# Kernel tuning notes

Measured on AMD Instinct MI355X. Metric: run time of the kernel, lower is better.

## Reference

```python
import jax, jax.numpy as jnp
import numpy as np

B, CDD, L, T, H, NH = 16, 10, 64, 128, 768, 12
DH = H // NH          # head dim = 64
S = CDD * L + T       # full sequence = 768 (640 candidate tokens + 128 terms)


def setup_inputs() -> dict:
    key = jax.random.key(0)
    ks = jax.random.split(key, 7)
    w = 0.02
    return {
        "hidden_states": jax.random.normal(ks[0], (B, S, H), jnp.float32),
        "Wq": jax.random.normal(ks[1], (H, H), jnp.float32) * w,
        "bq": jax.random.normal(ks[2], (H,), jnp.float32) * w,
        "Wk": jax.random.normal(ks[3], (H, H), jnp.float32) * w,
        "bk": jax.random.normal(ks[4], (H,), jnp.float32) * w,
        "Wv": jax.random.normal(ks[5], (H, H), jnp.float32) * w,
        "bv": jax.random.normal(ks[6], (H,), jnp.float32) * w,
    }


def _one_pass_mask(dtype):
    # block-diagonal over candidates + dense global columns for terms
    block = jnp.kron(jnp.eye(CDD, dtype=dtype), jnp.ones((L, L), dtype=dtype))  # [CDD*L, CDD*L]
    return jnp.concatenate([block, jnp.ones((CDD * L, T), dtype=dtype)], axis=-1)  # [CDD*L, S]


def reference(hidden_states, Wq, bq, Wk, bk, Wv, bv):
    def split_heads(x):  # [B, s, H] -> [B, NH, s, DH]
        return x.reshape(B, -1, NH, DH).transpose(0, 2, 1, 3)

    attn_field = hidden_states[:, :-T]                     # [B, CDD*L, H] queries only
    q = split_heads(attn_field @ Wq.T + bq)                # [B, NH, CDD*L, DH]
    k = split_heads(hidden_states @ Wk.T + bk)             # [B, NH, S, DH]
    v = split_heads(hidden_states @ Wv.T + bv)             # [B, NH, S, DH]

    mask = _one_pass_mask(q.dtype)                         # [CDD*L, S]
    scale = 1.0 / np.sqrt(DH).astype(np.float32)
    # NOTE: original multiplies scores by the mask (masked entries become 0, not -inf)
    scores = jnp.einsum('bhqd,bhkd->bhqk', q, k) * scale * mask
    probs = jax.nn.softmax(scores, axis=-1)                # [B, NH, CDD*L, S]

    ctx = jnp.einsum('bhqk,bhkd->bhqd', probs, v)          # [B, NH, CDD*L, DH]
    ctx = jnp.concatenate([ctx, v[:, :, -T:]], axis=2)     # append term values untouched
    return ctx.transpose(0, 2, 1, 3).reshape(B, S, H)
```

## Files before the change

### kernel.cpp

```cpp
#include <hip/hip_runtime.h>

constexpr int Bb  = 16;
constexpr int CDD = 10;
constexpr int Lc  = 64;
constexpr int T   = 128;
constexpr int H   = 768;
constexpr int NH  = 12;
constexpr int DH  = 64;
constexpr int S   = 768;
constexpr int SQ  = 640;
constexpr int MROWS = Bb * S;

typedef __attribute__((ext_vector_type(8))) short bf16x8;
typedef __attribute__((ext_vector_type(4))) short bf16x4;
typedef __attribute__((ext_vector_type(4))) float f32x4;

__device__ inline unsigned short f2bf(float f) {
  unsigned u = __float_as_uint(f);
  u += 0x7fff + ((u >> 16) & 1);
  return (unsigned short)(u >> 16);
}
__device__ inline float bf2f(unsigned short h) {
  return __uint_as_float(((unsigned)h) << 16);
}

__device__ inline void gld_lds16(const void* g, void* l) {
  __builtin_amdgcn_global_load_lds(
      (const __attribute__((address_space(1))) void*)g,
      (__attribute__((address_space(3))) void*)l, 16, 0, 0);
}

__device__ inline bf16x8 ld_b64x2(const unsigned short* p) {
  union { bf16x8 v; bf16x4 h[2]; } u;
  u.h[0] = *(const bf16x4*)p;
  u.h[1] = *(const bf16x4*)(p + 4);
  return u.v;
}

constexpr int NX4 = MROWS * H / 4;
constexpr int NW4 = H * H / 4;
__global__ void convert_all(const float* __restrict__ X,
                            const float* __restrict__ Wq,
                            const float* __restrict__ Wk,
                            const float* __restrict__ Wv,
                            unsigned short* __restrict__ Xb,
                            unsigned short* __restrict__ Wb,
                            float* __restrict__ part) {
  int i = blockIdx.x * blockDim.x + threadIdx.x;
  if (i < Bb * H) part[i] = 0.f;
  const int stride = gridDim.x * blockDim.x;
  const int total = NX4 + 3 * NW4;
  for (; i < total; i += stride) {
    const float* src;
    unsigned short* dst;
    int off;
    if (i < NX4) {
      src = X; dst = Xb; off = i;
    } else {
      int k = i - NX4;
      int w = k / NW4;
      off = k - w * NW4;
      src = (w == 0) ? Wq : (w == 1) ? Wk : Wv;
      dst = Wb + (size_t)w * H * H;
    }
    float4 v = ((const float4*)src)[off];
    ushort4 o;
    o.x = f2bf(v.x); o.y = f2bf(v.y); o.z = f2bf(v.z); o.w = f2bf(v.w);
    ((ushort4*)dst)[off] = o;
  }
}

__launch_bounds__(256, 4)
__global__ void qkv_gemm(const unsigned short* __restrict__ Xb,
                         const unsigned short* __restrict__ Wb,
                         const float* __restrict__ bq, const float* __restrict__ bk,
                         const float* __restrict__ bv,
                         unsigned short* __restrict__ Qb, unsigned short* __restrict__ Kb,
                         unsigned short* __restrict__ Vb,
                         float* __restrict__ part,
                         float* __restrict__ out) {
  const int z = blockIdx.z;
  if (z == 0 && (blockIdx.x % 6) == 5) return;
  const unsigned short* W = Wb + (size_t)z * H * H;
  const float* bias = (z == 0) ? bq : (z == 1) ? bk : bv;
  unsigned short* Y = (z == 0) ? Qb : (z == 1) ? Kb : Vb;

  const int i0 = blockIdx.x * 128;
  const int j0 = blockIdx.y * 128;
  const int tid = threadIdx.x;
  const int wave = tid >> 6, lane = tid & 63;
  const int wr = wave >> 1, wc = wave & 1;
  const int col = lane & 15, quad = lane >> 4;

  __shared__ unsigned short As[128 * 64];
  __shared__ unsigned short Bs[128 * 64];

  f32x4 acc[4][4];
#pragma unroll
  for (int i = 0; i < 4; i++)
#pragma unroll
    for (int j = 0; j < 4; j++) acc[i][j] = (f32x4){0.f, 0.f, 0.f, 0.f};

  int rS[4], gcS[4];
#pragma unroll
  for (int i = 0; i < 4; i++) {
    int s = tid + 256 * i;
    rS[i] = s >> 3;
    gcS[i] = (s & 7) ^ (rS[i] & 7);
  }

  for (int kt = 0; kt < 12; kt++) {
    const int k0 = kt * 64;
#pragma unroll
    for (int i = 0; i < 4; i++)
      gld_lds16(Xb + (size_t)(i0 + rS[i]) * H + k0 + gcS[i] * 8, &As[(tid + 256 * i) * 8]);
#pragma unroll
    for (int i = 0; i < 4; i++)
      gld_lds16(W + (size_t)(j0 + rS[i]) * H + k0 + gcS[i] * 8, &Bs[(tid + 256 * i) * 8]);
    __builtin_amdgcn_s_waitcnt(0);
    __syncthreads();

#pragma unroll
    for (int h = 0; h < 2; h++) {
      bf16x8 a[4], b[4];
#pragma unroll
      for (int mt = 0; mt < 4; mt++) {
        int r = wr * 64 + mt * 16 + col;
        a[mt] = *(const bf16x8*)&As[r * 64 + (((h * 4 + quad) ^ (r & 7)) * 8)];
      }
#pragma unroll
      for (int nt = 0; nt < 4; nt++) {
        int r = wc * 64 + nt * 16 + col;
        b[nt] = *(const bf16x8*)&Bs[r * 64 + (((h * 4 + quad) ^ (r & 7)) * 8)];
      }
#pragma unroll
      for (int mt = 0; mt < 4; mt++)
#pragma unroll
        for (int nt = 0; nt < 4; nt++)
          acc[mt][nt] = __builtin_amdgcn_mfma_f32_16x16x32_bf16(a[mt], b[nt], acc[mt][nt], 0, 0, 0);
    }
    __syncthreads();
  }

  float colsum[4] = {0.f, 0.f, 0.f, 0.f};
#pragma unroll
  for (int mt = 0; mt < 4; mt++) {
#pragma unroll
    for (int nt = 0; nt < 4; nt++) {
      const int j = j0 + wc * 64 + nt * 16 + col;
      const float bj = bias[j];
#pragma unroll
      for (int r = 0; r < 4; r++) {
        const int i = i0 + wr * 64 + mt * 16 + quad * 4 + r;
        const float v = acc[mt][nt][r] + bj;
        Y[(size_t)i * H + j] = f2bf(v);
        if (z == 2) {
          colsum[nt] += v;
          int s = i - (i / S) * S;
          if (s >= SQ) out[(size_t)i * H + j] = v;
        }
      }
    }
  }
  if (z == 2) {
    const int b = blockIdx.x / 6;
#pragma unroll
    for (int nt = 0; nt < 4; nt++) {
      float s = colsum[nt];
      s += __shfl_xor(s, 16, 64);
      s += __shfl_xor(s, 32, 64);
      if (quad == 0) {
        const int j = j0 + wc * 64 + nt * 16 + col;
        atomicAdd(&part[b * H + j], s);
      }
    }
  }
}

__launch_bounds__(256, 3)
__global__ void attn_kernel(const unsigned short* __restrict__ Qb,
                            const unsigned short* __restrict__ Kb,
                            const unsigned short* __restrict__ Vb,
                            const float* __restrict__ part,
                            float* __restrict__ out) {
  const int g = blockIdx.x;
  const int bid = (g & 7) * 240 + (g >> 3);
  const int c = bid % CDD;
  const int h = (bid / CDD) % NH;
  const int b = bid / (CDD * NH);
  const int tid = threadIdx.x;
  const int wave = tid >> 6, lane = tid & 63;
  const int col = lane & 15, quad = lane >> 4;

  __shared__ __align__(16) char smem[50176];
  unsigned short* Ks = (unsigned short*)smem;
  unsigned short* Ps = (unsigned short*)smem;
  unsigned short* Vt = (unsigned short*)(smem + 25088);

  const size_t rowQ0 = (size_t)(b * S + c * 64) * H + h * DH;

#pragma unroll
  for (int j = 0; j < 6; j++) {
    int s = tid + 256 * j;
    int key = s >> 3;
    int gkey = (key < 64) ? (c * 64 + key) : (576 + key);
    int gc = (s & 7) ^ (key & 7);
    gld_lds16(Kb + (size_t)(b * S + gkey) * H + h * DH + gc * 8, &Ks[s * 8]);
  }
  asm volatile("" ::: "memory");

  const int rq = wave * 16 + col;
  const unsigned short* qp = Qb + rowQ0 + (size_t)rq * H;
  bf16x8 a0 = *(const bf16x8*)(qp + quad * 8);
  bf16x8 a1 = *(const bf16x8*)(qp + 32 + quad * 8);
  asm volatile("" ::: "memory");

  int4 uv[6];
#pragma unroll
  for (int j = 0; j < 6; j++) {
    int s = tid + 256 * j;
    int key = s >> 3;
    int f0 = (s & 7) * 8;
    int gkey = (key < 64) ? (c * 64 + key) : (576 + key);
    uv[j] = *(const int4*)(Vb + (size_t)(b * S + gkey) * H + h * DH + f0);
  }
  asm volatile("s_waitcnt vmcnt(8)" ::: "memory");
  __builtin_amdgcn_sched_barrier(0);
  __builtin_amdgcn_s_barrier();
  __builtin_amdgcn_sched_barrier(0);

  f32x4 sc[12];
#pragma unroll
  for (int n = 0; n < 12; n++) sc[n] = (f32x4){0.f, 0.f, 0.f, 0.f};
#pragma unroll
  for (int n = 0; n < 12; n++) {
    const int rk = n * 16 + col;
    bf16x8 b0 = *(const bf16x8*)&Ks[rk * 64 + ((quad ^ (rk & 7)) * 8)];
    bf16x8 b1 = *(const bf16x8*)&Ks[rk * 64 + (((4 + quad) ^ (rk & 7)) * 8)];
    sc[n] = __builtin_amdgcn_mfma_f32_16x16x32_bf16(a0, b0, sc[n], 0, 0, 0);
    sc[n] = __builtin_amdgcn_mfma_f32_16x16x32_bf16(a1, b1, sc[n], 0, 0, 0);
  }

  float em[4], zin[4];
  {
    const float scale = 0.125f;
#pragma unroll
    for (int r = 0; r < 4; r++) {
      float mx = sc[0][r];
#pragma unroll
      for (int n = 1; n < 12; n++) mx = fmaxf(mx, sc[n][r]);
#pragma unroll
      for (int msk = 1; msk <= 8; msk <<= 1) mx = fmaxf(mx, __shfl_xor(mx, msk, 64));
      const float mrow = fmaxf(mx * scale, 0.f);
      float rs = 0.f;
#pragma unroll
      for (int n = 0; n < 12; n++) {
        float p = __expf(sc[n][r] * scale - mrow);
        sc[n][r] = p;
        rs += p;
      }
#pragma unroll
      for (int msk = 1; msk <= 8; msk <<= 1) rs += __shfl_xor(rs, msk, 64);
      const float e = __expf(-mrow);
      em[r] = e;
      zin[r] = 1.f / (rs + 576.f * e);
    }
  }
  __syncthreads();

#pragma unroll
  for (int n = 0; n < 12; n++)
#pragma unroll
    for (int r = 0; r < 4; r++)
      Ps[(wave * 16 + quad * 4 + r) * 196 + n * 16 + col] = f2bf(sc[n][r]);

#pragma unroll
  for (int j = 0; j < 6; j++) {
    int s = tid + 256 * j;
    int key = s >> 3;
    int f0 = (s & 7) * 8;
    union { int4 i4; unsigned short u[8]; } w;
    w.i4 = uv[j];
#pragma unroll
    for (int i = 0; i < 8; i++) Vt[(f0 + i) * 196 + key] = w.u[i];
  }
  __syncthreads();

  f32x4 o[4], osum[4];
#pragma unroll
  for (int n2 = 0; n2 < 4; n2++) {
    o[n2] = (f32x4){0.f, 0.f, 0.f, 0.f};
    osum[n2] = (f32x4){0.f, 0.f, 0.f, 0.f};
  }
  bf16x8 ones;
#pragma unroll
  for (int i = 0; i < 8; i++) ones[i] = (short)0x3F80;
#pragma unroll
  for (int ks = 0; ks < 6; ks++) {
    bf16x8 a = ld_b64x2(&Ps[(wave * 16 + col) * 196 + ks * 32 + quad * 8]);
#pragma unroll
    for (int n2 = 0; n2 < 4; n2++) {
      bf16x8 bvv = ld_b64x2(&Vt[(n2 * 16 + col) * 196 + ks * 32 + quad * 8]);
      o[n2] = __builtin_amdgcn_mfma_f32_16x16x32_bf16(a, bvv, o[n2], 0, 0, 0);
      osum[n2] = __builtin_amdgcn_mfma_f32_16x16x32_bf16(ones, bvv, osum[n2], 0, 0, 0);
    }
  }

#pragma unroll
  for (int n2 = 0; n2 < 4; n2++) {
    const int d = n2 * 16 + col;
    const float vc = part[b * H + h * DH + d] - osum[n2][0];
#pragma unroll
    for (int r = 0; r < 4; r++) {
      const int m = wave * 16 + quad * 4 + r;
      const float val = (o[n2][r] + em[r] * vc) * zin[r];
      out[(size_t)(b * S + c * 64 + m) * H + h * DH + d] = val;
    }
  }
}

extern "C" void kernel_launch(void* const* d_in, const int* in_sizes, int n_in,
                              void* d_out, int out_size, void* d_ws, size_t ws_size,
                              hipStream_t stream) {
  const float* X  = (const float*)d_in[0];
  const float* Wq = (const float*)d_in[1];
  const float* bq = (const float*)d_in[2];
  const float* Wk = (const float*)d_in[3];
  const float* bk = (const float*)d_in[4];
  const float* Wv = (const float*)d_in[5];
  const float* bv = (const float*)d_in[6];
  float* out = (float*)d_out;

  char* ws = (char*)d_ws;
  unsigned short* Xb   = (unsigned short*)ws;
  unsigned short* Wb   = (unsigned short*)(ws + 18874368);
  unsigned short* Qb   = (unsigned short*)(ws + 22413312);
  unsigned short* Kb   = (unsigned short*)(ws + 41287680);
  unsigned short* Vb   = (unsigned short*)(ws + 60162048);
  float*          part = (float*)(ws + 79036416);

  convert_all<<<2048, 256, 0, stream>>>(X, Wq, Wk, Wv, Xb, Wb, part);
  qkv_gemm<<<dim3(96, 6, 3), 256, 0, stream>>>(Xb, Wb, bq, bk, bv, Qb, Kb, Vb, part, out);
  attn_kernel<<<1920, 256, 0, stream>>>(Qb, Kb, Vb, part, out);
}
```

Baseline: 170.1 us.

## Process two candidates per attention block, reusing shared term K/V tiles

Each attention block now handles a pair of candidates instead of one, halving the grid. The 128 term-key K and V rows stay resident in LDS and only the candidate-specific 64 rows are reloaded for the second candidate. The second candidate's loads are issued before the first candidate's PV stage so they overlap with it. The cost is more LDS per block (separate K, P and V regions), lower occupancy (launch bound 3 to 2) and fewer blocks for load balancing.

```diff
diff --git a/kernel.cpp b/kernel.cpp
--- a/kernel.cpp
+++ b/kernel.cpp
@@ -177,52 +177,54 @@
   }
 }
 
-__launch_bounds__(256, 3)
+__launch_bounds__(256, 2)
 __global__ void attn_kernel(const unsigned short* __restrict__ Qb,
                             const unsigned short* __restrict__ Kb,
                             const unsigned short* __restrict__ Vb,
                             const float* __restrict__ part,
                             float* __restrict__ out) {
   const int g = blockIdx.x;
-  const int bid = (g & 7) * 240 + (g >> 3);
-  const int c = bid % CDD;
-  const int h = (bid / CDD) % NH;
-  const int b = bid / (CDD * NH);
+  const int bid = (g & 7) * 120 + (g >> 3);
+  const int cpair = bid % 5;
+  const int h = (bid / 5) % NH;
+  const int b = bid / (5 * NH);
+  const int c0 = cpair * 2;
+  const int c1 = c0 + 1;
   const int tid = threadIdx.x;
   const int wave = tid >> 6, lane = tid & 63;
   const int col = lane & 15, quad = lane >> 4;
 
-  __shared__ __align__(16) char smem[50176];
+  __shared__ __align__(16) char smem[74752];
   unsigned short* Ks = (unsigned short*)smem;
-  unsigned short* Ps = (unsigned short*)smem;
-  unsigned short* Vt = (unsigned short*)(smem + 25088);
-
-  const size_t rowQ0 = (size_t)(b * S + c * 64) * H + h * DH;
+  unsigned short* Ps = (unsigned short*)(smem + 24576);
+  unsigned short* Vt = (unsigned short*)(smem + 49664);
+
+  const float* ptot = part + b * H + h * DH;
+
+#define FENCE asm volatile("" ::: "memory")
 
 #pragma unroll
   for (int j = 0; j < 6; j++) {
     int s = tid + 256 * j;
     int key = s >> 3;
-    int gkey = (key < 64) ? (c * 64 + key) : (576 + key);
+    int gkey = (key < 64) ? (c0 * 64 + key) : (576 + key);
     int gc = (s & 7) ^ (key & 7);
     gld_lds16(Kb + (size_t)(b * S + gkey) * H + h * DH + gc * 8, &Ks[s * 8]);
   }
-  asm volatile("" ::: "memory");
-
+  FENCE;
   const int rq = wave * 16 + col;
-  const unsigned short* qp = Qb + rowQ0 + (size_t)rq * H;
-  bf16x8 a0 = *(const bf16x8*)(qp + quad * 8);
-  bf16x8 a1 = *(const bf16x8*)(qp + 32 + quad * 8);
-  asm volatile("" ::: "memory");
-
-  int4 uv[6];
+  const unsigned short* qp0 = Qb + (size_t)(b * S + c0 * 64 + rq) * H + h * DH;
+  bf16x8 a0 = *(const bf16x8*)(qp0 + quad * 8);
+  bf16x8 a1 = *(const bf16x8*)(qp0 + 32 + quad * 8);
+  FENCE;
+  int4 uv0[6];
 #pragma unroll
   for (int j = 0; j < 6; j++) {
     int s = tid + 256 * j;
     int key = s >> 3;
     int f0 = (s & 7) * 8;
-    int gkey = (key < 64) ? (c * 64 + key) : (576 + key);
-    uv[j] = *(const int4*)(Vb + (size_t)(b * S + gkey) * H + h * DH + f0);
+    int gkey = (key < 64) ? (c0 * 64 + key) : (576 + key);
+    uv0[j] = *(const int4*)(Vb + (size_t)(b * S + gkey) * H + h * DH + f0);
   }
   asm volatile("s_waitcnt vmcnt(8)" ::: "memory");
   __builtin_amdgcn_sched_barrier(0);
@@ -269,54 +271,169 @@
   __syncthreads();
 
 #pragma unroll
+  for (int j = 0; j < 2; j++) {
+    int s = tid + 256 * j;
+    int key = s >> 3;
+    int gc = (s & 7) ^ (key & 7);
+    gld_lds16(Kb + (size_t)(b * S + c1 * 64 + key) * H + h * DH + gc * 8, &Ks[s * 8]);
+  }
+  FENCE;
+  const unsigned short* qp1 = Qb + (size_t)(b * S + c1 * 64 + rq) * H + h * DH;
+  bf16x8 a0n = *(const bf16x8*)(qp1 + quad * 8);
+  bf16x8 a1n = *(const bf16x8*)(qp1 + 32 + quad * 8);
+  FENCE;
+  int4 uv1[2];
+#pragma unroll
+  for (int j = 0; j < 2; j++) {
+    int s = tid + 256 * j;
+    int key = s >> 3;
+    int f0 = (s & 7) * 8;
+    uv1[j] = *(const int4*)(Vb + (size_t)(b * S + c1 * 64 + key) * H + h * DH + f0);
+  }
+  FENCE;
+
+#pragma unroll
   for (int n = 0; n < 12; n++)
 #pragma unroll
     for (int r = 0; r < 4; r++)
       Ps[(wave * 16 + quad * 4 + r) * 196 + n * 16 + col] = f2bf(sc[n][r]);
-
 #pragma unroll
   for (int j = 0; j < 6; j++) {
     int s = tid + 256 * j;
     int key = s >> 3;
     int f0 = (s & 7) * 8;
     union { int4 i4; unsigned short u[8]; } w;
-    w.i4 = uv[j];
+    w.i4 = uv0[j];
 #pragma unroll
     for (int i = 0; i < 8; i++) Vt[(f0 + i) * 196 + key] = w.u[i];
   }
+  asm volatile("s_waitcnt lgkmcnt(0)" ::: "memory");
+  __builtin_amdgcn_sched_barrier(0);
+  __builtin_amdgcn_s_barrier();
+  __builtin_amdgcn_sched_barrier(0);
+
+  bf16x8 ones;
+#pragma unroll
+  for (int i = 0; i < 8; i++) ones[i] = (short)0x3F80;
+
+  {
+    f32x4 o[4], osum[4];
+#pragma unroll
+    for (int n2 = 0; n2 < 4; n2++) {
+      o[n2] = (f32x4){0.f, 0.f, 0.f, 0.f};
+      osum[n2] = (f32x4){0.f, 0.f, 0.f, 0.f};
+    }
+#pragma unroll
+    for (int ks = 0; ks < 6; ks++) {
+      bf16x8 a = ld_b64x2(&Ps[(wave * 16 + col) * 196 + ks * 32 + quad * 8]);
+#pragma unroll
+      for (int n2 = 0; n2 < 4; n2++) {
+        bf16x8 bvv = ld_b64x2(&Vt[(n2 * 16 + col) * 196 + ks * 32 + quad * 8]);
+        o[n2] = __builtin_amdgcn_mfma_f32_16x16x32_bf16(a, bvv, o[n2], 0, 0, 0);
+        osum[n2] = __builtin_amdgcn_mfma_f32_16x16x32_bf16(ones, bvv, osum[n2], 0, 0, 0);
+      }
+    }
+#pragma unroll
+    for (int n2 = 0; n2 < 4; n2++) {
+      const int d = n2 * 16 + col;
+      const float vc = ptot[d] - osum[n2][0];
+#pragma unroll
+      for (int r = 0; r < 4; r++) {
+        const int m = wave * 16 + quad * 4 + r;
+        const float val = (o[n2][r] + em[r] * vc) * zin[r];
+        out[(size_t)(b * S + c0 * 64 + m) * H + h * DH + d] = val;
+      }
+    }
+  }
+
+  asm volatile("s_waitcnt vmcnt(4)" ::: "memory");
+  __builtin_amdgcn_sched_barrier(0);
+  __builtin_amdgcn_s_barrier();
+  __builtin_amdgcn_sched_barrier(0);
+
+#pragma unroll
+  for (int n = 0; n < 12; n++) sc[n] = (f32x4){0.f, 0.f, 0.f, 0.f};
+#pragma unroll
+  for (int n = 0; n < 12; n++) {
+    const int rk = n * 16 + col;
+    bf16x8 b0 = *(const bf16x8*)&Ks[rk * 64 + ((quad ^ (rk & 7)) * 8)];
+    bf16x8 b1 = *(const bf16x8*)&Ks[rk * 64 + (((4 + quad) ^ (rk & 7)) * 8)];
+    sc[n] = __builtin_amdgcn_mfma_f32_16x16x32_bf16(a0n, b0, sc[n], 0, 0, 0);
+    sc[n] = __builtin_amdgcn_mfma_f32_16x16x32_bf16(a1n, b1, sc[n], 0, 0, 0);
+  }
+
+  {
+    const float scale = 0.125f;
+#pragma unroll
+    for (int r = 0; r < 4; r++) {
+      float mx = sc[0][r];
+#pragma unroll
+      for (int n = 1; n < 12; n++) mx = fmaxf(mx, sc[n][r]);
+#pragma unroll
+      for (int msk = 1; msk <= 8; msk <<= 1) mx = fmaxf(mx, __shfl_xor(mx, msk, 64));
+      const float mrow = fmaxf(mx * scale, 0.f);
+      float rs = 0.f;
+#pragma unroll
+      for (int n = 0; n < 12; n++) {
+        float p = __expf(sc[n][r] * scale - mrow);
+        sc[n][r] = p;
+        rs += p;
+      }
+#pragma unroll
+      for (int msk = 1; msk <= 8; msk <<= 1) rs += __shfl_xor(rs, msk, 64);
+      const float e = __expf(-mrow);
+      em[r] = e;
+      zin[r] = 1.f / (rs + 576.f * e);
+    }
+  }
+
+#pragma unroll
+  for (int n = 0; n < 12; n++)
+#pragma unroll
+    for (int r = 0; r < 4; r++)
+      Ps[(wave * 16 + quad * 4 + r) * 196 + n * 16 + col] = f2bf(sc[n][r]);
+#pragma unroll
+  for (int j = 0; j < 2; j++) {
+    int s = tid + 256 * j;
+    int key = s >> 3;
+    int f0 = (s & 7) * 8;
+    union { int4 i4; unsigned short u[8]; } w;
+    w.i4 = uv1[j];
+#pragma unroll
+    for (int i = 0; i < 8; i++) Vt[(f0 + i) * 196 + key] = w.u[i];
+  }
   __syncthreads();
 
-  f32x4 o[4], osum[4];
-#pragma unroll
-  for (int n2 = 0; n2 < 4; n2++) {
-    o[n2] = (f32x4){0.f, 0.f, 0.f, 0.f};
-    osum[n2] = (f32x4){0.f, 0.f, 0.f, 0.f};
-  }
-  bf16x8 ones;
-#pragma unroll
-  for (int i = 0; i < 8; i++) ones[i] = (short)0x3F80;
-#pragma unroll
-  for (int ks = 0; ks < 6; ks++) {
-    bf16x8 a = ld_b64x2(&Ps[(wave * 16 + col) * 196 + ks * 32 + quad * 8]);
+  {
+    f32x4 o[4], osum[4];
 #pragma unroll
     for (int n2 = 0; n2 < 4; n2++) {
-      bf16x8 bvv = ld_b64x2(&Vt[(n2 * 16 + col) * 196 + ks * 32 + quad * 8]);
-      o[n2] = __builtin_amdgcn_mfma_f32_16x16x32_bf16(a, bvv, o[n2], 0, 0, 0);
-      osum[n2] = __builtin_amdgcn_mfma_f32_16x16x32_bf16(ones, bvv, osum[n2], 0, 0, 0);
-    }
-  }
-
-#pragma unroll
-  for (int n2 = 0; n2 < 4; n2++) {
-    const int d = n2 * 16 + col;
-    const float vc = part[b * H + h * DH + d] - osum[n2][0];
-#pragma unroll
-    for (int r = 0; r < 4; r++) {
-      const int m = wave * 16 + quad * 4 + r;
-      const float val = (o[n2][r] + em[r] * vc) * zin[r];
-      out[(size_t)(b * S + c * 64 + m) * H + h * DH + d] = val;
-    }
-  }
+      o[n2] = (f32x4){0.f, 0.f, 0.f, 0.f};
+      osum[n2] = (f32x4){0.f, 0.f, 0.f, 0.f};
+    }
+#pragma unroll
+    for (int ks = 0; ks < 6; ks++) {
+      bf16x8 a = ld_b64x2(&Ps[(wave * 16 + col) * 196 + ks * 32 + quad * 8]);
+#pragma unroll
+      for (int n2 = 0; n2 < 4; n2++) {
+        bf16x8 bvv = ld_b64x2(&Vt[(n2 * 16 + col) * 196 + ks * 32 + quad * 8]);
+        o[n2] = __builtin_amdgcn_mfma_f32_16x16x32_bf16(a, bvv, o[n2], 0, 0, 0);
+        osum[n2] = __builtin_amdgcn_mfma_f32_16x16x32_bf16(ones, bvv, osum[n2], 0, 0, 0);
+      }
+    }
+#pragma unroll
+    for (int n2 = 0; n2 < 4; n2++) {
+      const int d = n2 * 16 + col;
+      const float vc = ptot[d] - osum[n2][0];
+#pragma unroll
+      for (int r = 0; r < 4; r++) {
+        const int m = wave * 16 + quad * 4 + r;
+        const float val = (o[n2][r] + em[r] * vc) * zin[r];
+        out[(size_t)(b * S + c1 * 64 + m) * H + h * DH + d] = val;
+      }
+    }
+  }
+#undef FENCE
 }
 
 extern "C" void kernel_launch(void* const* d_in, const int* in_sizes, int n_in,
@@ -341,5 +458,5 @@
 
   convert_all<<<2048, 256, 0, stream>>>(X, Wq, Wk, Wv, Xb, Wb, part);
   qkv_gemm<<<dim3(96, 6, 3), 256, 0, stream>>>(Xb, Wb, bq, bk, bv, Qb, Kb, Vb, part, out);
-  attn_kernel<<<1920, 256, 0, stream>>>(Qb, Kb, Vb, part, out);
-}
+  attn_kernel<<<960, 256, 0, stream>>>(Qb, Kb, Vb, part, out);
+}
```

Result: no change. 173.1 us (+1.8%).
